# Optimization experiments

Hardware: AMD Instinct MI355X
Metric: run time of the kernel (lower is better)

## Reference

```python
import jax, jax.numpy as jnp
import numpy as np

BSZ, SEQ, HID = 4, 2048, 2048
NH, NKV, HD = 16, 8, 128
SLOTS, MAXSEQ = 8, 4096
EPS = 1e-6
SCALE = HD ** -0.5


def rms_norm(x, w):
    # normalize over last dim (head_dim)
    var = jnp.mean(jnp.square(x), axis=-1, keepdims=True)
    return x * jax.lax.rsqrt(var + EPS) * w


def setup_inputs() -> dict:
    key = jax.random.key(0)
    ks = jax.random.split(key, 6)
    return {
        "hidden_states": jax.random.normal(ks[0], (BSZ, SEQ, HID), jnp.float32),
        "positions": jnp.tile(jnp.arange(SEQ, dtype=jnp.int32)[None, :], (BSZ, 1)),
        "k_cache": jnp.zeros((SLOTS, MAXSEQ, NKV, HD), jnp.float32),
        "v_cache": jnp.zeros((SLOTS, MAXSEQ, NKV, HD), jnp.float32),
        "slot_mapping": jnp.arange(BSZ, dtype=jnp.int32),
        "kv_start_indices": jnp.zeros((BSZ,), jnp.int32),
        "seq_lens": jnp.full((BSZ,), SEQ, jnp.int32),
        "qkv_w": jax.random.normal(ks[1], ((NH + 2 * NKV) * HD, HID), jnp.float32) * 0.02,
        "qkv_b": jax.random.normal(ks[2], ((NH + 2 * NKV) * HD,), jnp.float32) * 0.02,
        "o_w": jax.random.normal(ks[3], (HID, NH * HD), jnp.float32) * 0.02,
        "q_norm_w": jnp.ones((HD,), jnp.float32),
        "k_norm_w": jnp.ones((HD,), jnp.float32),
    }


def reference(hidden_states, positions, k_cache, v_cache, slot_mapping,
              kv_start_indices, seq_lens, qkv_w, qkv_b, o_w, q_norm_w, k_norm_w):
    bsz, seq_len, _ = hidden_states.shape
    qkv = jnp.einsum("bsh,oh->bso", hidden_states, qkv_w) + qkv_b
    q, k, v = jnp.split(qkv, [NH * HD, NH * HD + NKV * HD], axis=-1)
    q = rms_norm(q.reshape(bsz, seq_len, NH, HD), q_norm_w)
    k = rms_norm(k.reshape(bsz, seq_len, NKV, HD), k_norm_w)
    v = v.reshape(bsz, seq_len, NKV, HD)

    # paged KV cache scatter: cache[slot, start:start+seq] = k/v  (vectorized over batch)
    rows = kv_start_indices[:, None] + jnp.arange(seq_len)[None, :]  # [B,S]
    k_cache = k_cache.at[slot_mapping[:, None], rows].set(k)
    v_cache = v_cache.at[slot_mapping[:, None], rows].set(v)

    # prefill path (seq_len > 1): gather back up to max_l (= seq_len here, static)
    max_l = seq_len
    k_h = k_cache[slot_mapping, :max_l].transpose(0, 2, 1, 3)  # [B,Hkv,L,D]
    v_h = v_cache[slot_mapping, :max_l].transpose(0, 2, 1, 3)
    n_rep = NH // NKV
    if n_rep > 1:  # repeat_interleave over head dim (GQA)
        k_h = jnp.repeat(k_h, n_rep, axis=1)
        v_h = jnp.repeat(v_h, n_rep, axis=1)

    qh = q.transpose(0, 2, 1, 3)  # [B,H,S,D]
    scores = jnp.einsum("bhqd,bhkd->bhqk", qh, k_h) * SCALE
    causal = jnp.tril(jnp.ones((seq_len, max_l), bool))
    scores = jnp.where(causal[None, None], scores, -jnp.inf)
    attn = jax.nn.softmax(scores, axis=-1)
    out = jnp.einsum("bhqk,bhkd->bhqd", attn, v_h)
    out = out.transpose(0, 2, 1, 3).reshape(bsz, seq_len, NH * HD)
    return jnp.einsum("bso,ho->bsh", out, o_w)
```

## Files before the change

kernel.cpp:

```cpp
#include <hip/hip_runtime.h>
#include <hip/hip_bf16.h>
#include <stdint.h>

typedef unsigned short u16;
typedef __attribute__((ext_vector_type(8))) __bf16 bf16x8;
typedef __attribute__((ext_vector_type(4))) float f32x4;

#define EPSF 1e-6f
#define SCALE 0.08838834764831845f

__device__ __forceinline__ u16 f2bf(float f) {
    union { float f; uint32_t u; } a; a.f = f;
    uint32_t r = a.u + 0x7FFFu + ((a.u >> 16) & 1u);
    return (u16)(r >> 16);
}
__device__ __forceinline__ float bf2f(u16 u) {
    union { uint32_t u; float f; } a; a.u = ((uint32_t)u) << 16;
    return a.f;
}
__device__ __forceinline__ u16 f2bf_n(float f) {
    __hip_bfloat16 h = __float2bfloat16(f);
    return *reinterpret_cast<u16*>(&h);
}

__global__ __launch_bounds__(256) void cvt_f32_bf16_k(
    const float* __restrict__ in, u16* __restrict__ out, long n4)
{
    long i = (long)blockIdx.x * 256 + threadIdx.x;
    if (i >= n4) return;
    float4 v = ((const float4*)in)[i];
    ushort4 o;
    o.x = f2bf(v.x); o.y = f2bf(v.y); o.z = f2bf(v.z); o.w = f2bf(v.w);
    ((ushort4*)out)[i] = o;
}

__device__ __forceinline__ void gload16(const u16* g, u16* l) {
    __builtin_amdgcn_global_load_lds(
        (const __attribute__((address_space(1))) uint32_t*)g,
        (__attribute__((address_space(3))) uint32_t*)l, 16, 0, 0);
}

__global__ __launch_bounds__(512, 2) void gemm8_nt(
    const u16* __restrict__ A, const u16* __restrict__ B,
    const float* __restrict__ bias,
    float* __restrict__ Cf, u16* __restrict__ Cb,
    int M, int N, int K)
{
    __shared__ u16 As[2][256 * 64];
    __shared__ u16 Bs[2][256 * 64];

    const int t = threadIdx.x;
    const int lane = t & 63;
    const int g = lane >> 4, lr = lane & 15;
    const int w = t >> 6;
    const int wm = w >> 2, wn = w & 3;

    const int nwg = gridDim.x * gridDim.y;
    const int bid0 = blockIdx.y * gridDim.x + blockIdx.x;
    const int cpx = nwg >> 3;
    const int bids = (bid0 & 7) * cpx + (bid0 >> 3);
    const int bn = (bids % gridDim.x) * 256;
    const int bm = (bids / gridDim.x) * 256;
    const int NT = K >> 6;

    f32x4 z = {0.f, 0.f, 0.f, 0.f};
    f32x4 acc[8][4];
#pragma unroll
    for (int m = 0; m < 8; ++m)
#pragma unroll
        for (int n = 0; n < 4; ++n) acc[m][n] = z;

    auto STAGE2 = [&](int buf, int k0, int p) {
#pragma unroll
        for (int j = 0; j < 2; ++j) {
            int idx = p * 1024 + j * 512 + t;
            int ci = idx & 2047;
            int row = ci >> 3, slot = ci & 7;
            int csrc = slot ^ (row & 7);
            if (idx < 2048)
                gload16(A + (size_t)(bm + row) * K + k0 + csrc * 8, &As[buf][0] + ci * 8);
            else
                gload16(B + (size_t)(bn + row) * K + k0 + csrc * 8, &Bs[buf][0] + ci * 8);
        }
    };

    bf16x8 afr0[4][2], afr1[4][2];
    bf16x8 bf0[2][2], bf1[2][2];

#pragma unroll
    for (int p = 0; p < 4; ++p) STAGE2(0, 0, p);

    for (int kt = 0; kt < NT; ++kt) {
        const int cur = kt & 1;
        const int k0n = (kt + 1) << 6;
        const bool last = (kt == NT - 1);
        const char* Ab = (const char*)&As[cur][0];
        const char* Bb = (const char*)&Bs[cur][0];
        const int swz = (lr & 7) << 4;

        auto LDA = [&](bf16x8 (&dst)[4][2], int mbase) {
#pragma unroll
            for (int mi = 0; mi < 4; ++mi) {
                int row = wm * 128 + (mbase + mi) * 16 + lr;
#pragma unroll
                for (int kc = 0; kc < 2; ++kc)
                    dst[mi][kc] = *(const bf16x8*)(Ab + row * 128 + ((kc * 64 + g * 16) ^ swz));
            }
        };
        auto LDB = [&](bf16x8 (&dst)[2][2], int nbase) {
#pragma unroll
            for (int ni = 0; ni < 2; ++ni) {
                int row = wn * 64 + (nbase + ni) * 16 + lr;
#pragma unroll
                for (int kc = 0; kc < 2; ++kc)
                    dst[ni][kc] = *(const bf16x8*)(Bb + row * 128 + ((kc * 64 + g * 16) ^ swz));
            }
        };
        auto MMA = [&](bf16x8 (&amf)[4][2], int mf0, int nf0, bf16x8 (&bfr)[2][2]) {
            __builtin_amdgcn_s_setprio(1);
#pragma unroll
            for (int mi = 0; mi < 4; ++mi)
#pragma unroll
                for (int ni = 0; ni < 2; ++ni)
#pragma unroll
                    for (int kc = 0; kc < 2; ++kc)
                        acc[mf0 + mi][nf0 + ni] = __builtin_amdgcn_mfma_f32_16x16x32_bf16(
                            amf[mi][kc], bfr[ni][kc], acc[mf0 + mi][nf0 + ni], 0, 0, 0);
            __builtin_amdgcn_s_setprio(0);
        };

        if (!last) {
#pragma unroll
            for (int p = 0; p < 4; ++p) STAGE2(cur ^ 1, k0n, p);
            asm volatile("s_waitcnt vmcnt(8)" ::: "memory");
        } else {
            asm volatile("s_waitcnt vmcnt(0)" ::: "memory");
        }
        __builtin_amdgcn_s_barrier();
        __builtin_amdgcn_sched_barrier(0);

        LDA(afr0, 0); LDB(bf0, 0); LDB(bf1, 2);
        MMA(afr0, 0, 0, bf0);
        MMA(afr0, 0, 2, bf1);
        LDA(afr1, 4);
        MMA(afr1, 4, 2, bf1);
        MMA(afr1, 4, 0, bf0);

        __builtin_amdgcn_sched_barrier(0);
        __builtin_amdgcn_s_barrier();
    }

#pragma unroll
    for (int mf = 0; mf < 8; ++mf) {
#pragma unroll
        for (int nf = 0; nf < 4; ++nf) {
            int col = bn + wn * 64 + nf * 16 + lr;
            float bv = bias ? bias[col] : 0.f;
#pragma unroll
            for (int r = 0; r < 4; ++r) {
                int row = bm + wm * 128 + mf * 16 + g * 4 + r;
                float v = acc[mf][nf][r] + bv;
                if (Cf) Cf[(size_t)row * N + col] = v;
                else    Cb[(size_t)row * N + col] = f2bf(v);
            }
        }
    }
}

__global__ __launch_bounds__(256) void rmsnorm_k(
    u16* __restrict__ qkv, const float* __restrict__ qw, const float* __restrict__ kw)
{
    const int row = blockIdx.x;
    const int w = threadIdx.x >> 6, l = threadIdx.x & 63;
#pragma unroll
    for (int i = 0; i < 6; ++i) {
        int head = w + i * 4;
        const float* wt = (head < 16) ? qw : kw;
        u16* p = qkv + (size_t)row * 4096 + head * 128;
        uint32_t u = *(const uint32_t*)(p + l * 2);
        float x0 = bf2f((u16)(u & 0xFFFF));
        float x1 = bf2f((u16)(u >> 16));
        float ss = x0 * x0 + x1 * x1;
#pragma unroll
        for (int m = 1; m < 64; m <<= 1) ss += __shfl_xor(ss, m, 64);
        float inv = rsqrtf(ss * (1.0f / 128.0f) + EPSF);
        float r0 = x0 * inv * wt[l * 2];
        float r1 = x1 * inv * wt[l * 2 + 1];
        uint32_t o = (uint32_t)f2bf(r0) | ((uint32_t)f2bf(r1) << 16);
        *(uint32_t*)(p + l * 2) = o;
    }
}

__global__ __launch_bounds__(256) void vtrans_k(
    const u16* __restrict__ qkv, u16* __restrict__ vt)
{
    __shared__ u16 T[64 * 64];
    const int t = threadIdx.x;
    const int sx = blockIdx.x * 64;
    const int dy = blockIdx.y * 64;
    const int z  = blockIdx.z;
    const int b = z >> 3, hk = z & 7;
#pragma unroll
    for (int j = 0; j < 2; ++j) {
        int idx = t + j * 256;
        int r = idx >> 3, c8 = (idx & 7) * 8;
        uint4 v = *(const uint4*)(qkv + (size_t)(b * 2048 + sx + r) * 4096 + 3072 + hk * 128 + dy + c8);
        int slot = (c8 >> 3) ^ ((r ^ (r >> 3)) & 7);
        *(uint4*)(&T[r * 64 + slot * 8]) = v;
    }
    __syncthreads();
#pragma unroll
    for (int j = 0; j < 2; ++j) {
        int idx = t + j * 256;
        int rr = idx >> 3, cc8 = (idx & 7) * 8;
        u16 tmp[8];
#pragma unroll
        for (int i = 0; i < 8; ++i) {
            int row = cc8 + i;
            int slot = (rr >> 3) ^ ((row ^ (row >> 3)) & 7);
            tmp[i] = T[row * 64 + slot * 8 + (rr & 7)];
        }
        *(uint4*)(vt + ((size_t)z * 128 + dy + rr) * 2048 + sx + cc8) = *(uint4*)tmp;
    }
}

#define P_S 72

__global__ __launch_bounds__(256, 2) void attn5_k(
    const u16* __restrict__ qkv, const u16* __restrict__ vt,
    u16* __restrict__ aout)
{
    __shared__ u16 Kt[2][64 * 128];
    __shared__ u16 Vl[2][128 * 64];
    __shared__ u16 P[4][16 * P_S];

    const int t = threadIdx.x;
    const int lane = t & 63;
    const int w = t >> 6;
    const int g = lane >> 4, lr = lane & 15;
    const int pr = blockIdx.x, h = blockIdx.y, b = blockIdx.z;
    const int hk = h >> 1;
    const size_t rowb = (size_t)b * 2048;

    const u16* ksrc = qkv + rowb * 4096 + 2048 + hk * 128;
    const u16* vsrc = vt + (size_t)(b * 8 + hk) * 128 * 2048;

    bf16x8 ones8;
    {
        union { bf16x8 v; u16 e[8]; } on;
#pragma unroll
        for (int j = 0; j < 8; ++j) on.e[j] = 0x3F80;
        ones8 = on.v;
    }

    auto STAGE = [&](int buf, int kvb) {
#pragma unroll
        for (int j = 0; j < 4; ++j) {
            int idx = t + j * 256;
            {
                int row = idx >> 4, slot = idx & 15;
                int csrc = (slot & 8) | ((slot & 7) ^ (row & 7));
                gload16(ksrc + (size_t)(kvb + row) * 4096 + csrc * 8, &Kt[buf][0] + idx * 8);
            }
            {
                int row = idx >> 3, slot = idx & 7;
                int csrc = slot ^ (row & 7);
                gload16(vsrc + (size_t)row * 2048 + kvb + csrc * 8, &Vl[buf][0] + idx * 8);
            }
        }
    };

    for (int sub = 0; sub < 2; ++sub) {
        const int qt = sub ? 15 - pr : pr;
        const int qbase = qt * 128;
        const int nt = 2 * qt + 2;

        bf16x8 qf[2][4];
        {
            const u16* qp = qkv + (rowb + qbase + w * 32 + lr) * 4096 + h * 128;
#pragma unroll
            for (int sb = 0; sb < 2; ++sb)
#pragma unroll
                for (int c = 0; c < 4; ++c) {
                    union { bf16x8 v; u16 e[8]; } uq;
                    uq.v = *(const bf16x8*)(qp + sb * 16 * 4096 + c * 32 + g * 8);
#pragma unroll
                    for (int jj = 0; jj < 8; ++jj) uq.e[jj] = f2bf(bf2f(uq.e[jj]) * SCALE);
                    qf[sb][c] = uq.v;
                }
        }

        float m_r[2][4];
        f32x4 z = {0.f, 0.f, 0.f, 0.f};
        f32x4 l_acc[2];
        f32x4 o_acc[2][8];
#pragma unroll
        for (int sb = 0; sb < 2; ++sb) {
#pragma unroll
            for (int r = 0; r < 4; ++r) m_r[sb][r] = -INFINITY;
            l_acc[sb] = z;
#pragma unroll
            for (int d = 0; d < 8; ++d) o_acc[sb][d] = z;
        }

        __syncthreads();
        STAGE(0, 0);

        for (int kt = 0; kt < nt; ++kt) {
            const int cur = kt & 1;
            const int kvb = kt * 64;
            asm volatile("s_waitcnt vmcnt(0)" ::: "memory");
            __builtin_amdgcn_s_barrier();
            __builtin_amdgcn_sched_barrier(0);
            if (kt + 1 < nt) STAGE(cur ^ 1, kvb + 64);
            __builtin_amdgcn_sched_barrier(0);

            const u16* Kc = &Kt[cur][0];
            const u16* Vc = &Vl[cur][0];
            const bool active = !(kt == nt - 1 && w < 2);
            const bool near = (kt >= nt - 2);

            if (active) {
                f32x4 s[2][4];
                __builtin_amdgcn_s_setprio(1);
#pragma unroll
                for (int cb = 0; cb < 4; ++cb) {
                    int row = cb * 16 + lr;
                    s[0][cb] = z; s[1][cb] = z;
#pragma unroll
                    for (int c = 0; c < 4; ++c) {
                        int chunk = c * 4 + g;
                        int slot = (chunk & 8) | ((chunk & 7) ^ (row & 7));
                        bf16x8 kf = *(const bf16x8*)(&Kc[row * 128 + slot * 8]);
                        s[0][cb] = __builtin_amdgcn_mfma_f32_16x16x32_bf16(qf[0][c], kf, s[0][cb], 0, 0, 0);
                        s[1][cb] = __builtin_amdgcn_mfma_f32_16x16x32_bf16(qf[1][c], kf, s[1][cb], 0, 0, 0);
                    }
                }
                __builtin_amdgcn_s_setprio(0);

#pragma unroll
                for (int sb = 0; sb < 2; ++sb) {
#pragma unroll
                    for (int r = 0; r < 4; ++r) {
                        float v0 = s[sb][0][r], v1 = s[sb][1][r], v2 = s[sb][2][r], v3 = s[sb][3][r];
                        if (near) {
                            int qa = qbase + w * 32 + sb * 16 + g * 4 + r;
                            if (kvb + lr > qa)      v0 = -INFINITY;
                            if (kvb + 16 + lr > qa) v1 = -INFINITY;
                            if (kvb + 32 + lr > qa) v2 = -INFINITY;
                            if (kvb + 48 + lr > qa) v3 = -INFINITY;
                        }
                        float mx = fmaxf(fmaxf(v0, v1), fmaxf(v2, v3));
                        mx = fmaxf(mx, __shfl_xor(mx, 1));
                        mx = fmaxf(mx, __shfl_xor(mx, 2));
                        mx = fmaxf(mx, __shfl_xor(mx, 4));
                        mx = fmaxf(mx, __shfl_xor(mx, 8));
                        float mold = m_r[sb][r];
                        float mbase;
                        if (__all(mx <= mold + 8.0f)) {
                            mbase = mold;
                        } else {
                            float mnew = fmaxf(mold, mx);
                            float alpha = __expf(mold - mnew);
                            l_acc[sb][r] *= alpha;
#pragma unroll
                            for (int d = 0; d < 8; ++d) o_acc[sb][d][r] *= alpha;
                            m_r[sb][r] = mnew;
                            mbase = mnew;
                        }
                        float p0 = __expf(v0 - mbase), p1 = __expf(v1 - mbase);
                        float p2 = __expf(v2 - mbase), p3 = __expf(v3 - mbase);
                        int prow = (g * 4 + r) * P_S;
                        P[w][prow + lr]      = f2bf_n(p0);
                        P[w][prow + 16 + lr] = f2bf_n(p1);
                        P[w][prow + 32 + lr] = f2bf_n(p2);
                        P[w][prow + 48 + lr] = f2bf_n(p3);
                    }

#pragma unroll
                    for (int kk = 0; kk < 2; ++kk) {
                        bf16x8 pa = *(const bf16x8*)(&P[w][lr * P_S + kk * 32 + g * 8]);
                        __builtin_amdgcn_s_setprio(1);
                        l_acc[sb] = __builtin_amdgcn_mfma_f32_16x16x32_bf16(pa, ones8, l_acc[sb], 0, 0, 0);
#pragma unroll
                        for (int d = 0; d < 8; ++d) {
                            int row = d * 16 + lr;
                            int slot = (kk * 4 + g) ^ (row & 7);
                            bf16x8 vf = *(const bf16x8*)(&Vc[row * 64 + slot * 8]);
                            o_acc[sb][d] = __builtin_amdgcn_mfma_f32_16x16x32_bf16(pa, vf, o_acc[sb][d], 0, 0, 0);
                        }
                        __builtin_amdgcn_s_setprio(0);
                    }
                }
            }
            __builtin_amdgcn_sched_barrier(0);
        }

#pragma unroll
        for (int sb = 0; sb < 2; ++sb) {
            const int qrow0 = qbase + w * 32 + sb * 16 + g * 4;
#pragma unroll
            for (int r = 0; r < 4; ++r) {
                float inv = 1.0f / l_acc[sb][r];
                u16* op = aout + (rowb + qrow0 + r) * 2048 + h * 128;
#pragma unroll
                for (int d = 0; d < 8; ++d)
                    op[d * 16 + lr] = f2bf_n(o_acc[sb][d][r] * inv);
            }
        }
    }
}

extern "C" void kernel_launch(void* const* d_in, const int* in_sizes, int n_in,
                              void* d_out, int out_size, void* d_ws, size_t ws_size,
                              hipStream_t stream)
{
    const float* hidden = (const float*)d_in[0];
    const float* qkv_w = (const float*)d_in[7];
    const float* qkv_b = (const float*)d_in[8];
    const float* o_w   = (const float*)d_in[9];
    const float* q_nw  = (const float*)d_in[10];
    const float* k_nw  = (const float*)d_in[11];

    char* ws = (char*)d_ws;
    u16* hid_bf  = (u16*)ws; ws += (size_t)8192 * 2048 * 2;
    u16* wqkv_bf = (u16*)ws; ws += (size_t)4096 * 2048 * 2;
    u16* ow_bf   = (u16*)ws; ws += (size_t)2048 * 2048 * 2;
    u16* qkv_bf  = (u16*)ws; ws += (size_t)8192 * 4096 * 2;
    u16* attn_bf = (u16*)ws; ws += (size_t)8192 * 2048 * 2;
    u16* vt_bf   = hid_bf;

    cvt_f32_bf16_k<<<16384, 256, 0, stream>>>(hidden, hid_bf, 4194304L);
    cvt_f32_bf16_k<<<8192, 256, 0, stream>>>(qkv_w, wqkv_bf, 2097152L);
    cvt_f32_bf16_k<<<4096, 256, 0, stream>>>(o_w, ow_bf, 1048576L);

    gemm8_nt<<<dim3(16, 32), 512, 0, stream>>>(hid_bf, wqkv_bf, qkv_b,
                                               nullptr, qkv_bf, 8192, 4096, 2048);
    rmsnorm_k<<<dim3(8192), 256, 0, stream>>>(qkv_bf, q_nw, k_nw);
    vtrans_k<<<dim3(32, 2, 32), 256, 0, stream>>>(qkv_bf, vt_bf);
    attn5_k<<<dim3(8, 16, 4), 256, 0, stream>>>(qkv_bf, vt_bf, attn_bf);
    gemm8_nt<<<dim3(8, 32), 512, 0, stream>>>(attn_bf, ow_bf, nullptr,
                                              (float*)d_out, nullptr, 8192, 2048, 2048);
}
```

Measured before the change: 413.5 us.

## Fuse QK RMSNorm into QKV GEMM epilogue and merge conversion kernels

The per-head RMSNorm is computed inside the QKV GEMM epilogue. Row sums of squares are reduced across lanes and across the two wave columns that share a 128-wide head through shared memory, then applied before the bf16 store. This removes a separate kernel that re-read and re-wrote the whole QKV buffer. The three fp32-to-bf16 conversion launches are also merged into one, relying on the workspace buffers being contiguous. The epilogue now adds a barrier and LDS reuse, and rounding changes slightly because it normalizes fp32 values before the single bf16 conversion.

```diff
diff --git a/kernel.cpp b/kernel.cpp
--- a/kernel.cpp
+++ b/kernel.cpp
@@ -23,12 +23,18 @@
     return *reinterpret_cast<u16*>(&h);
 }
 
-__global__ __launch_bounds__(256) void cvt_f32_bf16_k(
-    const float* __restrict__ in, u16* __restrict__ out, long n4)
+__global__ __launch_bounds__(256) void cvt_all_k(
+    const float* __restrict__ a,
+    const float* __restrict__ b,
+    const float* __restrict__ c,
+    u16* __restrict__ out)
 {
     long i = (long)blockIdx.x * 256 + threadIdx.x;
-    if (i >= n4) return;
-    float4 v = ((const float4*)in)[i];
+    const float* src; long off;
+    if (i < 4194304L)      { src = a; off = 0; }
+    else if (i < 6291456L) { src = b; off = 4194304L; }
+    else                   { src = c; off = 6291456L; }
+    float4 v = ((const float4*)src)[i - off];
     ushort4 o;
     o.x = f2bf(v.x); o.y = f2bf(v.y); o.z = f2bf(v.z); o.w = f2bf(v.w);
     ((ushort4*)out)[i] = o;
@@ -44,7 +50,8 @@
     const u16* __restrict__ A, const u16* __restrict__ B,
     const float* __restrict__ bias,
     float* __restrict__ Cf, u16* __restrict__ Cb,
-    int M, int N, int K)
+    int M, int N, int K,
+    const float* __restrict__ qnw, const float* __restrict__ knw, int fuse_rms)
 {
     __shared__ u16 As[2][256 * 64];
     __shared__ u16 Bs[2][256 * 64];
@@ -150,44 +157,63 @@
         __builtin_amdgcn_s_barrier();
     }
 
-#pragma unroll
-    for (int mf = 0; mf < 8; ++mf) {
-#pragma unroll
-        for (int nf = 0; nf < 4; ++nf) {
-            int col = bn + wn * 64 + nf * 16 + lr;
-            float bv = bias ? bias[col] : 0.f;
+    if (Cb && fuse_rms) {
+#pragma unroll
+        for (int mf = 0; mf < 8; ++mf)
+#pragma unroll
+            for (int nf = 0; nf < 4; ++nf) {
+                float bv = bias[bn + wn * 64 + nf * 16 + lr];
+#pragma unroll
+                for (int r = 0; r < 4; ++r) acc[mf][nf][r] += bv;
+            }
+        float* S = (float*)&As[0][0];
+#pragma unroll
+        for (int mf = 0; mf < 8; ++mf)
 #pragma unroll
             for (int r = 0; r < 4; ++r) {
+                float ps = 0.f;
+#pragma unroll
+                for (int nf = 0; nf < 4; ++nf) ps += acc[mf][nf][r] * acc[mf][nf][r];
+                ps += __shfl_xor(ps, 1);
+                ps += __shfl_xor(ps, 2);
+                ps += __shfl_xor(ps, 4);
+                ps += __shfl_xor(ps, 8);
+                if (lr == 0) S[(wm * 4 + wn) * 128 + mf * 16 + g * 4 + r] = ps;
+            }
+        __syncthreads();
+        const int head = (bn + wn * 64) >> 7;
+        const bool isq = head < 16, isk = !isq && head < 24;
+#pragma unroll
+        for (int mf = 0; mf < 8; ++mf)
+#pragma unroll
+            for (int r = 0; r < 4; ++r) {
+                int rl = mf * 16 + g * 4 + r;
+                float tot = S[(wm * 4 + wn) * 128 + rl] + S[(wm * 4 + (wn ^ 1)) * 128 + rl];
+                float inv = (isq || isk) ? rsqrtf(tot * (1.0f / 128.0f) + EPSF) : 1.0f;
                 int row = bm + wm * 128 + mf * 16 + g * 4 + r;
-                float v = acc[mf][nf][r] + bv;
-                if (Cf) Cf[(size_t)row * N + col] = v;
-                else    Cb[(size_t)row * N + col] = f2bf(v);
-            }
-        }
-    }
-}
-
-__global__ __launch_bounds__(256) void rmsnorm_k(
-    u16* __restrict__ qkv, const float* __restrict__ qw, const float* __restrict__ kw)
-{
-    const int row = blockIdx.x;
-    const int w = threadIdx.x >> 6, l = threadIdx.x & 63;
-#pragma unroll
-    for (int i = 0; i < 6; ++i) {
-        int head = w + i * 4;
-        const float* wt = (head < 16) ? qw : kw;
-        u16* p = qkv + (size_t)row * 4096 + head * 128;
-        uint32_t u = *(const uint32_t*)(p + l * 2);
-        float x0 = bf2f((u16)(u & 0xFFFF));
-        float x1 = bf2f((u16)(u >> 16));
-        float ss = x0 * x0 + x1 * x1;
-#pragma unroll
-        for (int m = 1; m < 64; m <<= 1) ss += __shfl_xor(ss, m, 64);
-        float inv = rsqrtf(ss * (1.0f / 128.0f) + EPSF);
-        float r0 = x0 * inv * wt[l * 2];
-        float r1 = x1 * inv * wt[l * 2 + 1];
-        uint32_t o = (uint32_t)f2bf(r0) | ((uint32_t)f2bf(r1) << 16);
-        *(uint32_t*)(p + l * 2) = o;
+#pragma unroll
+                for (int nf = 0; nf < 4; ++nf) {
+                    int col = bn + wn * 64 + nf * 16 + lr;
+                    float wt = isq ? qnw[col & 127] : (isk ? knw[col & 127] : 1.0f);
+                    Cb[(size_t)row * N + col] = f2bf_n(acc[mf][nf][r] * inv * wt);
+                }
+            }
+    } else {
+#pragma unroll
+        for (int mf = 0; mf < 8; ++mf) {
+#pragma unroll
+            for (int nf = 0; nf < 4; ++nf) {
+                int col = bn + wn * 64 + nf * 16 + lr;
+                float bv = bias ? bias[col] : 0.f;
+#pragma unroll
+                for (int r = 0; r < 4; ++r) {
+                    int row = bm + wm * 128 + mf * 16 + g * 4 + r;
+                    float v = acc[mf][nf][r] + bv;
+                    if (Cf) Cf[(size_t)row * N + col] = v;
+                    else    Cb[(size_t)row * N + col] = f2bf(v);
+                }
+            }
+        }
     }
 }
 
@@ -430,15 +456,14 @@
     u16* attn_bf = (u16*)ws; ws += (size_t)8192 * 2048 * 2;
     u16* vt_bf   = hid_bf;
 
-    cvt_f32_bf16_k<<<16384, 256, 0, stream>>>(hidden, hid_bf, 4194304L);
-    cvt_f32_bf16_k<<<8192, 256, 0, stream>>>(qkv_w, wqkv_bf, 2097152L);
-    cvt_f32_bf16_k<<<4096, 256, 0, stream>>>(o_w, ow_bf, 1048576L);
+    cvt_all_k<<<28672, 256, 0, stream>>>(hidden, qkv_w, o_w, hid_bf);
 
     gemm8_nt<<<dim3(16, 32), 512, 0, stream>>>(hid_bf, wqkv_bf, qkv_b,
-                                               nullptr, qkv_bf, 8192, 4096, 2048);
-    rmsnorm_k<<<dim3(8192), 256, 0, stream>>>(qkv_bf, q_nw, k_nw);
+                                               nullptr, qkv_bf, 8192, 4096, 2048,
+                                               q_nw, k_nw, 1);
     vtrans_k<<<dim3(32, 2, 32), 256, 0, stream>>>(qkv_bf, vt_bf);
     attn5_k<<<dim3(8, 16, 4), 256, 0, stream>>>(qkv_bf, vt_bf, attn_bf);
     gemm8_nt<<<dim3(8, 32), 512, 0, stream>>>(attn_bf, ow_bf, nullptr,
-                                              (float*)d_out, nullptr, 8192, 2048, 2048);
-}
+                                              (float*)d_out, nullptr, 8192, 2048, 2048,
+                                              nullptr, nullptr, 0);
+}
```

After: 421.3 us. About the same (+1.9%).
